# Kernel optimization log

Hardware: AMD Instinct MI355X
Metric: run time of the kernel (lower is better)

Reference implementation:

```python
import jax, jax.numpy as jnp
import numpy as np

NU = 100000
NV = 100000
D = 128
R = 5          # num_support (rating levels)
O = 64         # output_dim // num_support
E = 640000     # edges per relation


def setup_inputs() -> dict:
    key = jax.random.key(0)
    ks = jax.random.split(key, 7)
    x_u = jax.random.normal(ks[0], (NU, D), dtype=jnp.float32)
    x_v = jax.random.normal(ks[1], (NV, D), dtype=jnp.float32)
    sup_rows = jax.random.randint(ks[2], (R, E), 0, NU, dtype=jnp.int32)
    sup_cols = jax.random.randint(ks[3], (R, E), 0, NV, dtype=jnp.int32)
    sup_vals = jax.random.uniform(ks[4], (R, E), dtype=jnp.float32)
    weights_u = jax.random.normal(ks[5], (R, D, O), dtype=jnp.float32)
    weights_v = jax.random.normal(ks[6], (R, D, O), dtype=jnp.float32)
    return {"x_u": x_u, "x_v": x_v, "sup_rows": sup_rows, "sup_cols": sup_cols,
            "sup_vals": sup_vals, "weights_u": weights_u, "weights_v": weights_v}


def _spmm(rows, cols, vals, feat, num_segments):
    # sparse [num_segments, n_src] @ feat [n_src, O] via gather + segment_sum
    return jax.ops.segment_sum(vals[:, None] * feat[cols], rows,
                               num_segments=num_segments)


def reference(x_u, x_v, sup_rows, sup_cols, sup_vals, weights_u, weights_v):
    # ordinal weight accumulation: wu_i = sum_{j<=i} weights_u[j]
    Wu = jnp.cumsum(weights_u, axis=0)  # [R, D, O]
    Wv = jnp.cumsum(weights_v, axis=0)  # [R, D, O]
    tmp_u = jnp.einsum('nd,rdo->rno', x_u, Wu)  # [R, NU, O]
    tmp_v = jnp.einsum('md,rdo->rmo', x_v, Wv)  # [R, NV, O]
    # z_u = sum_r support[r] @ tmp_v[r];  z_v = sum_r support[r]^T @ tmp_u[r]
    z_u = jax.vmap(lambda r, c, v, f: _spmm(r, c, v, f, NU))(
        sup_rows, sup_cols, sup_vals, tmp_v).sum(axis=0)
    z_v = jax.vmap(lambda r, c, v, f: _spmm(r, c, v, f, NV))(
        sup_cols, sup_rows, sup_vals, tmp_u).sum(axis=0)
    return jax.nn.relu(z_u), jax.nn.relu(z_v)
```

## Files before the change

kernel.cpp:

```cpp
#include <hip/hip_runtime.h>
#include <hip/hip_bf16.h>

#define R_SUP 5
#define D_IN 128
#define O_OUT 64
#define NBMAX 512
#define CHUNK 8192

typedef __attribute__((ext_vector_type(8))) short bf16x8;
typedef __attribute__((ext_vector_type(8))) unsigned short u16x8;
typedef __attribute__((ext_vector_type(4))) float f32x4;

__device__ __forceinline__ unsigned short f2bf(float f) {
  union { float f; unsigned int u; } c; c.f = f;
  unsigned int u = c.u;
  return (unsigned short)((u + 0x7FFFu + ((u >> 16) & 1u)) >> 16);
}
__device__ __forceinline__ float bf2f(unsigned short h) {
  return __uint_as_float(((unsigned int)h) << 16);
}

__global__ __launch_bounds__(256) void cumsum_w(
    const float* __restrict__ wu, const float* __restrict__ wv,
    float* __restrict__ wcu, float* __restrict__ wcv,
    unsigned short* __restrict__ wtbu, unsigned short* __restrict__ wtbv) {
  int i = blockIdx.x * 256 + threadIdx.x;
  if (i >= D_IN * O_OUT) return;
  const int d = i >> 6;
  const int o = i & 63;
  float su = 0.f, sv = 0.f;
#pragma unroll
  for (int r = 0; r < R_SUP; ++r) {
    su += wu[r * D_IN * O_OUT + i];
    sv += wv[r * D_IN * O_OUT + i];
    wcu[r * D_IN * O_OUT + i] = su;
    wcv[r * D_IN * O_OUT + i] = sv;
    wtbu[((size_t)r * O_OUT + o) * D_IN + d] = f2bf(su);
    wtbv[((size_t)r * O_OUT + o) * D_IN + d] = f2bf(sv);
  }
}

__global__ __launch_bounds__(256) void zero_f32(float* __restrict__ p, int n4) {
  int i = blockIdx.x * 256 + threadIdx.x;
  int stride = gridDim.x * 256;
  float4 z = make_float4(0.f, 0.f, 0.f, 0.f);
  for (; i < n4; i += stride) ((float4*)p)[i] = z;
}

__global__ __launch_bounds__(256) void zero_i32(int* __restrict__ p, int n) {
  int i = blockIdx.x * 256 + threadIdx.x;
  int stride = gridDim.x * 256;
  for (; i < n; i += stride) p[i] = 0;
}

__global__ __launch_bounds__(256) void gemm5_mfma(
    const float* __restrict__ x,
    const unsigned short* __restrict__ wtb,
    unsigned short* __restrict__ tmp5, size_t strideR, int N) {
  __shared__ unsigned short st[64][72];
  const int tid = threadIdx.x;
  const int row0 = blockIdx.x * 64;
  const int wave = tid >> 6;
  const int lane = tid & 63;
  const int m = lane & 15;
  const int q = lane >> 4;
  const int o0 = wave * 16;

  bf16x8 a[4][4];
#pragma unroll
  for (int rt = 0; rt < 4; ++rt) {
    int row = row0 + rt * 16 + m;
    if (row >= N) row = N - 1;
    const float* px = x + (size_t)row * D_IN + q * 8;
#pragma unroll
    for (int k0 = 0; k0 < 4; ++k0) {
      float4 f0 = *(const float4*)(px + k0 * 32);
      float4 f1 = *(const float4*)(px + k0 * 32 + 4);
      bf16x8 t;
      t[0] = (short)f2bf(f0.x); t[1] = (short)f2bf(f0.y);
      t[2] = (short)f2bf(f0.z); t[3] = (short)f2bf(f0.w);
      t[4] = (short)f2bf(f1.x); t[5] = (short)f2bf(f1.y);
      t[6] = (short)f2bf(f1.z); t[7] = (short)f2bf(f1.w);
      a[rt][k0] = t;
    }
  }

  const int rr = tid >> 2;
  const int c0 = (tid & 3) * 16;

  for (int r = 0; r < R_SUP; ++r) {
    bf16x8 b[4];
    const unsigned short* pw =
        wtb + ((size_t)r * O_OUT + o0 + m) * D_IN + q * 8;
#pragma unroll
    for (int k0 = 0; k0 < 4; ++k0)
      b[k0] = *(const bf16x8*)(pw + k0 * 32);
#pragma unroll
    for (int rt = 0; rt < 4; ++rt) {
      f32x4 acc = {0.f, 0.f, 0.f, 0.f};
#pragma unroll
      for (int k0 = 0; k0 < 4; ++k0)
        acc = __builtin_amdgcn_mfma_f32_16x16x32_bf16(a[rt][k0], b[k0], acc,
                                                      0, 0, 0);
#pragma unroll
      for (int reg = 0; reg < 4; ++reg)
        st[rt * 16 + q * 4 + reg][o0 + m] = f2bf(acc[reg]);
    }
    __syncthreads();
    if (row0 + rr < N) {
      unsigned short* pz = tmp5 + (size_t)r * strideR + (size_t)row0 * O_OUT;
      *(int4*)(pz + rr * O_OUT + c0) = *(const int4*)&st[rr][c0];
      *(int4*)(pz + rr * O_OUT + c0 + 8) = *(const int4*)&st[rr][c0 + 8];
    }
    __syncthreads();
  }
}

__global__ __launch_bounds__(256) void coarse_hist(
    const int* __restrict__ rows, const int* __restrict__ cols,
    int* __restrict__ cnt_u, int* __restrict__ cnt_v, int nE5,
    int nbu, int nbv) {
  __shared__ int hu[NBMAX], hv[NBMAX];
  const int tid = threadIdx.x;
  for (int t = tid; t < NBMAX; t += 256) { hu[t] = 0; hv[t] = 0; }
  __syncthreads();
  const int n4 = nE5 >> 2;
  int i = blockIdx.x * 256 + tid;
  int stride = gridDim.x * 256;
  for (; i < n4; i += stride) {
    int4 rr = ((const int4*)rows)[i];
    int4 cc = ((const int4*)cols)[i];
    atomicAdd(&hu[rr.x >> 8], 1); atomicAdd(&hu[rr.y >> 8], 1);
    atomicAdd(&hu[rr.z >> 8], 1); atomicAdd(&hu[rr.w >> 8], 1);
    atomicAdd(&hv[cc.x >> 8], 1); atomicAdd(&hv[cc.y >> 8], 1);
    atomicAdd(&hv[cc.z >> 8], 1); atomicAdd(&hv[cc.w >> 8], 1);
  }
  for (i = (n4 << 2) + blockIdx.x * 256 + tid; i < nE5; i += stride) {
    atomicAdd(&hu[rows[i] >> 8], 1);
    atomicAdd(&hv[cols[i] >> 8], 1);
  }
  __syncthreads();
  for (int t = tid; t < nbu; t += 256) if (hu[t]) atomicAdd(&cnt_u[t], hu[t]);
  for (int t = tid; t < nbv; t += 256) if (hv[t]) atomicAdd(&cnt_v[t], hv[t]);
}

__global__ __launch_bounds__(512) void coarse_scan(
    int* __restrict__ cnt_u, int* __restrict__ cnt_v,
    int* __restrict__ cb_u, int* __restrict__ cb_v,
    int* __restrict__ gcur_u, int* __restrict__ gcur_v, int nbu, int nbv) {
  int* cnt = blockIdx.x ? cnt_v : cnt_u;
  int* cb  = blockIdx.x ? cb_v  : cb_u;
  int* gc  = blockIdx.x ? gcur_v : gcur_u;
  int nb   = blockIdx.x ? nbv   : nbu;
  __shared__ int sc[NBMAX];
  const int t = threadIdx.x;
  sc[t] = (t < nb) ? cnt[t] : 0;
  __syncthreads();
  for (int off = 1; off < NBMAX; off <<= 1) {
    int add = (t >= off) ? sc[t - off] : 0;
    __syncthreads();
    sc[t] += add;
    __syncthreads();
  }
  int excl = t ? sc[t - 1] : 0;
  if (t < nb) { cb[t] = excl; gc[t] = excl; }
  if (t == 0) cb[nb] = sc[NBMAX - 1];
}

__global__ __launch_bounds__(512) void coarse_scatter(
    const int* __restrict__ rows, const int* __restrict__ cols,
    const float* __restrict__ vals, int* __restrict__ gcur_u,
    int* __restrict__ gcur_v, int2* __restrict__ mid_u,
    int2* __restrict__ mid_v, int nE5, int E, int nbu, int nbv) {
  __shared__ int2 buf[CHUNK];
  __shared__ int h[NBMAX], sc[NBMAX], gb[NBMAX], cur[NBMAX];
  const int tid = threadIdx.x;
  const int dir = blockIdx.x & 1;
  const int base = (blockIdx.x >> 1) * CHUNK;
  const int end = min(base + CHUNK, nE5);
  const int E2 = 2 * E, E3 = 3 * E, E4 = 4 * E;

  const int* ids   = dir ? cols : rows;
  const int* other = dir ? rows : cols;
  int* gcur = dir ? gcur_v : gcur_u;
  int2* mid = dir ? mid_v : mid_u;
  const int nb = dir ? nbv : nbu;

  h[tid] = 0;
  __syncthreads();
  for (int i = base + tid; i < end; i += 512)
    atomicAdd(&h[ids[i] >> 8], 1);
  __syncthreads();
  sc[tid] = h[tid];
  __syncthreads();
  for (int off = 1; off < NBMAX; off <<= 1) {
    int add = (tid >= off) ? sc[tid - off] : 0;
    __syncthreads();
    sc[tid] += add;
    __syncthreads();
  }
  int excl = tid ? sc[tid - 1] : 0;
  cur[tid] = excl;
  if (tid < nb && h[tid]) gb[tid] = atomicAdd(&gcur[tid], h[tid]);
  __syncthreads();
  for (int i = base + tid; i < end; i += 512) {
    int id = ids[i];
    int src = other[i];
    int vb = __float_as_int(vals[i]);
    int r = (i >= E) + (i >= E2) + (i >= E3) + (i >= E4);
    int pos = atomicAdd(&cur[id >> 8], 1);
    buf[pos] = make_int2(((id & 255) << 20) | (r << 17) | src, vb);
  }
  __syncthreads();
  const int wv = tid >> 6;
  const int lane = tid & 63;
  for (int b = wv; b < nb; b += 8) {
    int s = b ? sc[b - 1] : 0;
    int e = sc[b];
    if (s == e) continue;
    int2* dst = mid + gb[b];
    for (int j = s + lane; j < e; j += 64) dst[j - s] = buf[j];
  }
}

__global__ __launch_bounds__(256) void fine_scatter(
    const int2* __restrict__ mid, const int* __restrict__ cb,
    int* __restrict__ rp, int2* __restrict__ fin, int nbuck, int Ndst,
    int strideR) {
  __shared__ int h[256], sc[256], cur[256];
  const int tid = threadIdx.x;
  const int b = blockIdx.x;
  const int s = cb[b];
  const int e2 = cb[b + 1];
  h[tid] = 0;
  __syncthreads();
  for (int i = s + tid; i < e2; i += 256)
    atomicAdd(&h[(mid[i].x >> 20) & 255], 1);
  __syncthreads();
  sc[tid] = h[tid];
  __syncthreads();
  for (int off = 1; off < 256; off <<= 1) {
    int add = (tid >= off) ? sc[tid - off] : 0;
    __syncthreads();
    sc[tid] += add;
    __syncthreads();
  }
  int excl = tid ? sc[tid - 1] : 0;
  int d = b * 256 + tid;
  if (d <= Ndst) rp[d] = s + excl;
  if (b == nbuck - 1 && tid == 0 && Ndst >= nbuck * 256) rp[Ndst] = cb[nbuck];
  cur[tid] = s + excl;
  __syncthreads();
  for (int i = s + tid; i < e2; i += 256) {
    int2 pk = mid[i];
    int dl = (pk.x >> 20) & 255;
    int r = (pk.x >> 17) & 7;
    int src = pk.x & 0x1FFFF;
    int pos = atomicAdd(&cur[dl], 1);
    fin[pos] = make_int2(r * strideR + (src << 6), pk.y);
  }
}

__global__ __launch_bounds__(256) void spmm_pull_bf16(
    const int* __restrict__ rp, const int2* __restrict__ ep,
    const unsigned short* __restrict__ tmp5,
    float* __restrict__ z, int Ndst) {
  int g = (blockIdx.x * 256 + threadIdx.x) >> 3;
  int lane = threadIdx.x & 7;
  if (g >= Ndst) return;
  int s = rp[g];
  int e = rp[g + 1];
  const unsigned short* tl = tmp5 + lane * 8;
  float acc[8] = {0.f, 0.f, 0.f, 0.f, 0.f, 0.f, 0.f, 0.f};
  int i = s;
  for (; i + 8 <= e; i += 8) {
    int2 pk[8];
#pragma unroll
    for (int j = 0; j < 8; ++j) pk[j] = ep[i + j];
    u16x8 h[8];
#pragma unroll
    for (int j = 0; j < 8; ++j)
      h[j] = *(const u16x8*)(tl + (unsigned)pk[j].x);
#pragma unroll
    for (int j = 0; j < 8; ++j) {
      float v = __int_as_float(pk[j].y);
#pragma unroll
      for (int k = 0; k < 8; ++k) acc[k] += v * bf2f(h[j][k]);
    }
  }
  for (; i < e; ++i) {
    int2 pk = ep[i];
    float v = __int_as_float(pk.y);
    u16x8 h = *(const u16x8*)(tl + (unsigned)pk.x);
#pragma unroll
    for (int k = 0; k < 8; ++k) acc[k] += v * bf2f(h[k]);
  }
  float* zp = z + (size_t)g * O_OUT + lane * 8;
  float4 o0, o1;
  o0.x = fmaxf(acc[0], 0.f); o0.y = fmaxf(acc[1], 0.f);
  o0.z = fmaxf(acc[2], 0.f); o0.w = fmaxf(acc[3], 0.f);
  o1.x = fmaxf(acc[4], 0.f); o1.y = fmaxf(acc[5], 0.f);
  o1.z = fmaxf(acc[6], 0.f); o1.w = fmaxf(acc[7], 0.f);
  *(float4*)(zp) = o0;
  *(float4*)(zp + 4) = o1;
}

__global__ __launch_bounds__(256) void gemm64(
    const float* __restrict__ x, const float* __restrict__ w,
    float* __restrict__ out, int N) {
  __shared__ float sXT[D_IN][68];
  __shared__ float sW[D_IN][O_OUT];
  const int tid = threadIdx.x;
  const int row0 = blockIdx.x * 64;
  for (int i = tid; i < 2048; i += 256) {
    int d = i >> 4;
    int o4 = i & 15;
    ((float4*)&sW[d][0])[o4] = ((const float4*)w)[i];
  }
  for (int i = tid; i < 2048; i += 256) {
    int rl = i >> 5;
    int d4 = i & 31;
    int row = row0 + rl;
    float4 xv = make_float4(0.f, 0.f, 0.f, 0.f);
    if (row < N) xv = ((const float4*)x)[(size_t)row * 32 + d4];
    sXT[d4 * 4 + 0][rl] = xv.x;
    sXT[d4 * 4 + 1][rl] = xv.y;
    sXT[d4 * 4 + 2][rl] = xv.z;
    sXT[d4 * 4 + 3][rl] = xv.w;
  }
  __syncthreads();
  const int col4 = (tid & 15) * 4;
  const int row4 = (tid >> 4) * 4;
  float acc[4][4] = {};
#pragma unroll 8
  for (int d = 0; d < D_IN; ++d) {
    float4 xv = *(const float4*)&sXT[d][row4];
    float4 wv = *(const float4*)&sW[d][col4];
    acc[0][0] += xv.x * wv.x; acc[0][1] += xv.x * wv.y; acc[0][2] += xv.x * wv.z; acc[0][3] += xv.x * wv.w;
    acc[1][0] += xv.y * wv.x; acc[1][1] += xv.y * wv.y; acc[1][2] += xv.y * wv.z; acc[1][3] += xv.y * wv.w;
    acc[2][0] += xv.z * wv.x; acc[2][1] += xv.z * wv.y; acc[2][2] += xv.z * wv.z; acc[2][3] += xv.z * wv.w;
    acc[3][0] += xv.w * wv.x; acc[3][1] += xv.w * wv.y; acc[3][2] += xv.w * wv.z; acc[3][3] += xv.w * wv.w;
  }
#pragma unroll
  for (int i = 0; i < 4; ++i) {
    int row = row0 + row4 + i;
    if (row < N)
      *(float4*)&out[row * O_OUT + col4] =
          make_float4(acc[i][0], acc[i][1], acc[i][2], acc[i][3]);
  }
}

__global__ __launch_bounds__(256) void spmm_push(
    const int* __restrict__ dst, const int* __restrict__ src,
    const float* __restrict__ vals, const float* __restrict__ tmp,
    float* __restrict__ z, int E) {
  int t = blockIdx.x * 256 + threadIdx.x;
  int e = t >> 4;
  int lane = t & 15;
  if (e >= E) return;
  int d_ = dst[e];
  int s_ = src[e];
  float v = vals[e];
  float4 f = ((const float4*)tmp)[s_ * 16 + lane];
  float* zp = z + (size_t)d_ * O_OUT + lane * 4;
  atomicAdd(zp + 0, v * f.x);
  atomicAdd(zp + 1, v * f.y);
  atomicAdd(zp + 2, v * f.z);
  atomicAdd(zp + 3, v * f.w);
}

__global__ __launch_bounds__(256) void relu_f32(float* __restrict__ p, int n4) {
  int i = blockIdx.x * 256 + threadIdx.x;
  int stride = gridDim.x * 256;
  for (; i < n4; i += stride) {
    float4 v = ((float4*)p)[i];
    v.x = v.x > 0.f ? v.x : 0.f;
    v.y = v.y > 0.f ? v.y : 0.f;
    v.z = v.z > 0.f ? v.z : 0.f;
    v.w = v.w > 0.f ? v.w : 0.f;
    ((float4*)p)[i] = v;
  }
}

extern "C" void kernel_launch(void* const* d_in, const int* in_sizes, int n_in,
                              void* d_out, int out_size, void* d_ws, size_t ws_size,
                              hipStream_t stream) {
  const float* x_u      = (const float*)d_in[0];
  const float* x_v      = (const float*)d_in[1];
  const int*   sup_rows = (const int*)d_in[2];
  const int*   sup_cols = (const int*)d_in[3];
  const float* sup_vals = (const float*)d_in[4];
  const float* wu       = (const float*)d_in[5];
  const float* wv       = (const float*)d_in[6];

  const int NU = in_sizes[0] / D_IN;
  const int NV = in_sizes[1] / D_IN;
  const int E  = in_sizes[2] / R_SUP;
  const int Nmax = NU > NV ? NU : NV;
  const int nE5 = R_SUP * E;
  const int nbu = (NU + 255) / 256;
  const int nbv = (NV + 255) / 256;
  const int nbmax = nbu > nbv ? nbu : nbv;

  float* out = (float*)d_out;
  float* z_u = out;
  float* z_v = out + (size_t)NU * O_OUT;

  const int WDO = R_SUP * D_IN * O_OUT;
  const size_t strideR = (size_t)Nmax * O_OUT;
  const size_t bpad = (size_t)nbmax + 16;

  const size_t mid_bytes = (((size_t)nE5 * 8) + 255) & ~(size_t)255;

  const size_t needR = mid_bytes + (size_t)nE5 * 16 + strideR * R_SUP * 2 +
                       (size_t)2 * WDO * 4 + (size_t)2 * WDO * 2 +
                       ((size_t)Nmax + 16) * 4 + 6 * bpad * 4 + 512;

  if (ws_size >= needR && nbmax <= NBMAX && Nmax < (1 << 17)) {
    char* base = (char*)d_ws;
    int2* mid_u = (int2*)base;
    int2* mid_v = (int2*)(base + mid_bytes);
    int2* fin   = mid_v + nE5;
    unsigned short* tmp5 = (unsigned short*)(fin + nE5);
    float* wcu = (float*)(tmp5 + strideR * R_SUP);
    float* wcv = wcu + WDO;
    unsigned short* wtbu = (unsigned short*)(wcv + WDO);
    unsigned short* wtbv = wtbu + WDO;
    int* rp    = (int*)(wtbv + WDO);
    int* cnt_u = rp + Nmax + 16;
    int* cnt_v = cnt_u + bpad;
    int* cb_u  = cnt_v + bpad;
    int* cb_v  = cb_u + bpad;
    int* gcur_u = cb_v + bpad;
    int* gcur_v = gcur_u + bpad;

    cumsum_w<<<(D_IN * O_OUT + 255) / 256, 256, 0, stream>>>(
        wu, wv, wcu, wcv, wtbu, wtbv);
    zero_i32<<<(2 * (int)bpad + 255) / 256, 256, 0, stream>>>(cnt_u, 2 * (int)bpad);
    coarse_hist<<<512, 256, 0, stream>>>(sup_rows, sup_cols, cnt_u, cnt_v,
                                         nE5, nbu, nbv);
    coarse_scan<<<2, 512, 0, stream>>>(cnt_u, cnt_v, cb_u, cb_v, gcur_u,
                                       gcur_v, nbu, nbv);
    coarse_scatter<<<2 * ((nE5 + CHUNK - 1) / CHUNK), 512, 0, stream>>>(
        sup_rows, sup_cols, sup_vals, gcur_u, gcur_v, mid_u, mid_v, nE5, E,
        nbu, nbv);

    fine_scatter<<<nbu, 256, 0, stream>>>(mid_u, cb_u, rp, fin, nbu, NU,
                                          (int)strideR);
    gemm5_mfma<<<(NV + 63) / 64, 256, 0, stream>>>(x_v, wtbv, tmp5, strideR, NV);
    spmm_pull_bf16<<<(NU * 8 + 255) / 256, 256, 0, stream>>>(
        rp, fin, tmp5, z_u, NU);

    fine_scatter<<<nbv, 256, 0, stream>>>(mid_v, cb_v, rp, fin, nbv, NV,
                                          (int)strideR);
    gemm5_mfma<<<(NU + 63) / 64, 256, 0, stream>>>(x_u, wtbu, tmp5, strideR, NU);
    spmm_pull_bf16<<<(NV * 8 + 255) / 256, 256, 0, stream>>>(
        rp, fin, tmp5, z_v, NV);
  } else {
    float* wcu = (float*)d_ws;
    float* wcv = wcu + WDO;
    unsigned short* wtbu = (unsigned short*)(wcv + WDO);
    unsigned short* wtbv = wtbu + WDO;
    float* tmp = (float*)(wtbv + WDO);
    const int n4_out = out_size / 4;
    cumsum_w<<<(D_IN * O_OUT + 255) / 256, 256, 0, stream>>>(
        wu, wv, wcu, wcv, wtbu, wtbv);
    zero_f32<<<1024, 256, 0, stream>>>(out, n4_out);
    const int spmm_blocks = (E * 16 + 255) / 256;
    for (int r = 0; r < R_SUP; ++r) {
      const int* rws = sup_rows + (size_t)r * E;
      const int* cls = sup_cols + (size_t)r * E;
      const float* vls = sup_vals + (size_t)r * E;
      gemm64<<<(NV + 63) / 64, 256, 0, stream>>>(x_v, wcv + r * D_IN * O_OUT, tmp, NV);
      spmm_push<<<spmm_blocks, 256, 0, stream>>>(rws, cls, vls, tmp, z_u, E);
      gemm64<<<(NU + 63) / 64, 256, 0, stream>>>(x_u, wcu + r * D_IN * O_OUT, tmp, NU);
      spmm_push<<<spmm_blocks, 256, 0, stream>>>(cls, rws, vls, tmp, z_v, E);
    }
    relu_f32<<<1024, 256, 0, stream>>>(out, n4_out);
  }
}
```

Measured before the change: 556.2 us.

## Fuse fine scatter into SpMM using LDS-staged per-bucket sort

Removes the separate fine_scatter kernel and the global fin/rp arrays. Each 512-thread block now sorts its coarse bucket's edges by destination inside LDS, in chunks of up to FCAP entries, and then accumulates the gathered bf16 rows directly from the shared buffer. This avoids a global write and re-read of the sorted edge list plus two launches. In exchange it uses a large shared buffer (about 72KB) per block, which lowers occupancy, runs only 391 blocks per pass, and uses 16 lanes per row with 4-wide gathers instead of 8-wide.

```diff
diff --git a/kernel.cpp b/kernel.cpp
--- a/kernel.cpp
+++ b/kernel.cpp
@@ -6,9 +6,9 @@
 #define O_OUT 64
 #define NBMAX 512
 #define CHUNK 8192
+#define FCAP 9216
 
 typedef __attribute__((ext_vector_type(8))) short bf16x8;
-typedef __attribute__((ext_vector_type(8))) unsigned short u16x8;
 typedef __attribute__((ext_vector_type(4))) float f32x4;
 
 __device__ __forceinline__ unsigned short f2bf(float f) {
@@ -223,86 +223,99 @@
   }
 }
 
-__global__ __launch_bounds__(256) void fine_scatter(
+__global__ __launch_bounds__(512) void spmm_sorted(
     const int2* __restrict__ mid, const int* __restrict__ cb,
-    int* __restrict__ rp, int2* __restrict__ fin, int nbuck, int Ndst,
-    int strideR) {
+    const unsigned short* __restrict__ tmp5, float* __restrict__ z,
+    int Ndst, int strideR) {
+  __shared__ int2 buf[FCAP];
   __shared__ int h[256], sc[256], cur[256];
   const int tid = threadIdx.x;
   const int b = blockIdx.x;
   const int s = cb[b];
-  const int e2 = cb[b + 1];
-  h[tid] = 0;
-  __syncthreads();
-  for (int i = s + tid; i < e2; i += 256)
-    atomicAdd(&h[(mid[i].x >> 20) & 255], 1);
-  __syncthreads();
-  sc[tid] = h[tid];
-  __syncthreads();
-  for (int off = 1; off < 256; off <<= 1) {
-    int add = (tid >= off) ? sc[tid - off] : 0;
-    __syncthreads();
-    sc[tid] += add;
-    __syncthreads();
-  }
-  int excl = tid ? sc[tid - 1] : 0;
-  int d = b * 256 + tid;
-  if (d <= Ndst) rp[d] = s + excl;
-  if (b == nbuck - 1 && tid == 0 && Ndst >= nbuck * 256) rp[Ndst] = cb[nbuck];
-  cur[tid] = s + excl;
-  __syncthreads();
-  for (int i = s + tid; i < e2; i += 256) {
-    int2 pk = mid[i];
-    int dl = (pk.x >> 20) & 255;
-    int r = (pk.x >> 17) & 7;
-    int src = pk.x & 0x1FFFF;
-    int pos = atomicAdd(&cur[dl], 1);
-    fin[pos] = make_int2(r * strideR + (src << 6), pk.y);
-  }
-}
-
-__global__ __launch_bounds__(256) void spmm_pull_bf16(
-    const int* __restrict__ rp, const int2* __restrict__ ep,
-    const unsigned short* __restrict__ tmp5,
-    float* __restrict__ z, int Ndst) {
-  int g = (blockIdx.x * 256 + threadIdx.x) >> 3;
-  int lane = threadIdx.x & 7;
-  if (g >= Ndst) return;
-  int s = rp[g];
-  int e = rp[g + 1];
-  const unsigned short* tl = tmp5 + lane * 8;
-  float acc[8] = {0.f, 0.f, 0.f, 0.f, 0.f, 0.f, 0.f, 0.f};
-  int i = s;
-  for (; i + 8 <= e; i += 8) {
-    int2 pk[8];
-#pragma unroll
-    for (int j = 0; j < 8; ++j) pk[j] = ep[i + j];
-    u16x8 h[8];
-#pragma unroll
-    for (int j = 0; j < 8; ++j)
-      h[j] = *(const u16x8*)(tl + (unsigned)pk[j].x);
-#pragma unroll
-    for (int j = 0; j < 8; ++j) {
-      float v = __int_as_float(pk[j].y);
-#pragma unroll
-      for (int k = 0; k < 8; ++k) acc[k] += v * bf2f(h[j][k]);
-    }
-  }
-  for (; i < e; ++i) {
-    int2 pk = ep[i];
-    float v = __int_as_float(pk.y);
-    u16x8 h = *(const u16x8*)(tl + (unsigned)pk.x);
-#pragma unroll
-    for (int k = 0; k < 8; ++k) acc[k] += v * bf2f(h[k]);
-  }
-  float* zp = z + (size_t)g * O_OUT + lane * 8;
-  float4 o0, o1;
-  o0.x = fmaxf(acc[0], 0.f); o0.y = fmaxf(acc[1], 0.f);
-  o0.z = fmaxf(acc[2], 0.f); o0.w = fmaxf(acc[3], 0.f);
-  o1.x = fmaxf(acc[4], 0.f); o1.y = fmaxf(acc[5], 0.f);
-  o1.z = fmaxf(acc[6], 0.f); o1.w = fmaxf(acc[7], 0.f);
-  *(float4*)(zp) = o0;
-  *(float4*)(zp + 4) = o1;
+  const int e = cb[b + 1];
+  const int d0 = b * 256;
+  const int gid = tid >> 4;
+  const int lane = tid & 15;
+  const unsigned short* tl = tmp5 + lane * 4;
+
+  float4 acc[8];
+#pragma unroll
+  for (int k = 0; k < 8; ++k) acc[k] = make_float4(0.f, 0.f, 0.f, 0.f);
+
+  for (int cs = s; cs < e; cs += FCAP) {
+    const int ce = min(cs + FCAP, e);
+    if (tid < 256) h[tid] = 0;
+    __syncthreads();
+    for (int i = cs + tid; i < ce; i += 512)
+      atomicAdd(&h[(mid[i].x >> 20) & 255], 1);
+    __syncthreads();
+    if (tid < 256) sc[tid] = h[tid];
+    __syncthreads();
+    for (int off = 1; off < 256; off <<= 1) {
+      int add = (tid < 256 && tid >= off) ? sc[tid - off] : 0;
+      __syncthreads();
+      if (tid < 256) sc[tid] += add;
+      __syncthreads();
+    }
+    if (tid < 256) cur[tid] = tid ? sc[tid - 1] : 0;
+    __syncthreads();
+    for (int i = cs + tid; i < ce; i += 512) {
+      int2 pk = mid[i];
+      int dl = (pk.x >> 20) & 255;
+      int r = (pk.x >> 17) & 7;
+      int src = pk.x & 0x1FFFF;
+      int pos = atomicAdd(&cur[dl], 1);
+      buf[pos] = make_int2(r * strideR + (src << 6), pk.y);
+    }
+    __syncthreads();
+#pragma unroll
+    for (int k = 0; k < 8; ++k) {
+      const int dl = gid + (k << 5);
+      int i = dl ? sc[dl - 1] : 0;
+      const int re = sc[dl];
+      float4 a = acc[k];
+      for (; i + 8 <= re; i += 8) {
+        int2 pk[8];
+#pragma unroll
+        for (int j = 0; j < 8; ++j) pk[j] = buf[i + j];
+        ushort4 hh[8];
+#pragma unroll
+        for (int j = 0; j < 8; ++j)
+          hh[j] = *(const ushort4*)(tl + (unsigned)pk[j].x);
+#pragma unroll
+        for (int j = 0; j < 8; ++j) {
+          float v = __int_as_float(pk[j].y);
+          a.x += v * bf2f(hh[j].x);
+          a.y += v * bf2f(hh[j].y);
+          a.z += v * bf2f(hh[j].z);
+          a.w += v * bf2f(hh[j].w);
+        }
+      }
+      for (; i < re; ++i) {
+        int2 pk = buf[i];
+        float v = __int_as_float(pk.y);
+        ushort4 hh = *(const ushort4*)(tl + (unsigned)pk.x);
+        a.x += v * bf2f(hh.x);
+        a.y += v * bf2f(hh.y);
+        a.z += v * bf2f(hh.z);
+        a.w += v * bf2f(hh.w);
+      }
+      acc[k] = a;
+    }
+    __syncthreads();
+  }
+#pragma unroll
+  for (int k = 0; k < 8; ++k) {
+    int d = d0 + gid + (k << 5);
+    if (d < Ndst) {
+      float4 o;
+      o.x = fmaxf(acc[k].x, 0.f);
+      o.y = fmaxf(acc[k].y, 0.f);
+      o.z = fmaxf(acc[k].z, 0.f);
+      o.w = fmaxf(acc[k].w, 0.f);
+      ((float4*)(z + (size_t)d * O_OUT))[lane] = o;
+    }
+  }
 }
 
 __global__ __launch_bounds__(256) void gemm64(
@@ -412,22 +425,20 @@
 
   const size_t mid_bytes = (((size_t)nE5 * 8) + 255) & ~(size_t)255;
 
-  const size_t needR = mid_bytes + (size_t)nE5 * 16 + strideR * R_SUP * 2 +
+  const size_t needR = 2 * mid_bytes + strideR * R_SUP * 2 +
                        (size_t)2 * WDO * 4 + (size_t)2 * WDO * 2 +
-                       ((size_t)Nmax + 16) * 4 + 6 * bpad * 4 + 512;
+                       6 * bpad * 4 + 512;
 
   if (ws_size >= needR && nbmax <= NBMAX && Nmax < (1 << 17)) {
     char* base = (char*)d_ws;
     int2* mid_u = (int2*)base;
     int2* mid_v = (int2*)(base + mid_bytes);
-    int2* fin   = mid_v + nE5;
-    unsigned short* tmp5 = (unsigned short*)(fin + nE5);
+    unsigned short* tmp5 = (unsigned short*)(base + 2 * mid_bytes);
     float* wcu = (float*)(tmp5 + strideR * R_SUP);
     float* wcv = wcu + WDO;
     unsigned short* wtbu = (unsigned short*)(wcv + WDO);
     unsigned short* wtbv = wtbu + WDO;
-    int* rp    = (int*)(wtbv + WDO);
-    int* cnt_u = rp + Nmax + 16;
+    int* cnt_u = (int*)(wtbv + WDO);
     int* cnt_v = cnt_u + bpad;
     int* cb_u  = cnt_v + bpad;
     int* cb_v  = cb_u + bpad;
@@ -445,17 +456,13 @@
         sup_rows, sup_cols, sup_vals, gcur_u, gcur_v, mid_u, mid_v, nE5, E,
         nbu, nbv);
 
-    fine_scatter<<<nbu, 256, 0, stream>>>(mid_u, cb_u, rp, fin, nbu, NU,
-                                          (int)strideR);
     gemm5_mfma<<<(NV + 63) / 64, 256, 0, stream>>>(x_v, wtbv, tmp5, strideR, NV);
-    spmm_pull_bf16<<<(NU * 8 + 255) / 256, 256, 0, stream>>>(
-        rp, fin, tmp5, z_u, NU);
-
-    fine_scatter<<<nbv, 256, 0, stream>>>(mid_v, cb_v, rp, fin, nbv, NV,
-                                          (int)strideR);
+    spmm_sorted<<<nbu, 512, 0, stream>>>(mid_u, cb_u, tmp5, z_u, NU,
+                                         (int)strideR);
+
     gemm5_mfma<<<(NU + 63) / 64, 256, 0, stream>>>(x_u, wtbu, tmp5, strideR, NU);
-    spmm_pull_bf16<<<(NV * 8 + 255) / 256, 256, 0, stream>>>(
-        rp, fin, tmp5, z_v, NV);
+    spmm_sorted<<<nbv, 512, 0, stream>>>(mid_v, cb_v, tmp5, z_v, NV,
+                                         (int)strideR);
   } else {
     float* wcu = (float*)d_ws;
     float* wcv = wcu + WDO;
```

Result: faster. 471.8 us (-15.2%).
